# Optimization experiments

Measured on AMD Instinct MI355X. Metric: run time of the kernel, lower is better.

## Reference

```python
import jax, jax.numpy as jnp
import numpy as np

D_MODEL = 1024
NUM_HEADS = 16
D_K = D_MODEL // NUM_HEADS


def setup_inputs() -> dict:
    key = jax.random.key(0)
    ks = jax.random.split(key, 10)
    s = 1.0 / np.sqrt(D_MODEL)  # ~ torch Linear init scale
    inp = {
        "x": jax.random.normal(ks[0], (2, 2048, D_MODEL), dtype=jnp.float32),
        "Wq": jax.random.uniform(ks[1], (D_MODEL, D_MODEL), jnp.float32, -s, s),
        "bq": jax.random.uniform(ks[2], (D_MODEL,), jnp.float32, -s, s),
        "Wk": jax.random.uniform(ks[3], (D_MODEL, D_MODEL), jnp.float32, -s, s),
        "bk": jax.random.uniform(ks[4], (D_MODEL,), jnp.float32, -s, s),
        "Wv": jax.random.uniform(ks[5], (D_MODEL, D_MODEL), jnp.float32, -s, s),
        "bv": jax.random.uniform(ks[6], (D_MODEL,), jnp.float32, -s, s),
        "Wo": jax.random.uniform(ks[7], (D_MODEL, D_MODEL), jnp.float32, -s, s),
        "bo": jax.random.uniform(ks[8], (D_MODEL,), jnp.float32, -s, s),
        "ln_gamma": jnp.ones((D_MODEL,), jnp.float32),
        "ln_beta": jnp.zeros((D_MODEL,), jnp.float32),
    }
    return inp


def reference(x, Wq, bq, Wk, bk, Wv, bv, Wo, bo, ln_gamma, ln_beta):
    B, S, D = x.shape
    residual = x
    # LayerNorm (eps=1e-5 as torch default)
    mu = jnp.mean(x, axis=-1, keepdims=True)
    var = jnp.mean(jnp.square(x - mu), axis=-1, keepdims=True)
    xn = (x - mu) * jax.lax.rsqrt(var + 1e-5) * ln_gamma + ln_beta
    # QKV projections (torch Linear: y = x @ W^T + b) -> (B, H, S, d_k)
    def proj(W, b):
        return (xn @ W.T + b).reshape(B, S, NUM_HEADS, D_K).transpose(0, 2, 1, 3)
    Q, K, V = proj(Wq, bq), proj(Wk, bk), proj(Wv, bv)
    scores = jnp.einsum("bhqd,bhkd->bhqk", Q, K) / np.sqrt(D_K).astype(np.float32)
    attn = jax.nn.softmax(scores, axis=-1)  # (B, H, S, S); dropout is no-op (eval)
    context = jnp.einsum("bhqk,bhkd->bhqd", attn, V)
    context = context.transpose(0, 2, 1, 3).reshape(B, S, D)
    out = context @ Wo.T + bo
    return out + residual, attn.mean(axis=1)
```

## Files before the change

kernel.cpp:

```cpp
#include <hip/hip_runtime.h>
#include <stdint.h>
#include <stddef.h>

#define DEV static __device__ __forceinline__

typedef float f32x4 __attribute__((ext_vector_type(4)));
typedef float f32x16 __attribute__((ext_vector_type(16)));
typedef unsigned u32x4 __attribute__((ext_vector_type(4)));
typedef __bf16 bf16x8 __attribute__((ext_vector_type(8)));

DEV short f2bf(float f) {
  union { float f; unsigned u; } a; a.f = f;
  unsigned r = a.u + 0x7fffu + ((a.u >> 16) & 1u);
  return (short)(r >> 16);
}

DEV void gld_lds16(const void* g, void* lds) {
  __builtin_amdgcn_global_load_lds(
      (__attribute__((address_space(1))) void*)(void*)g,
      (__attribute__((address_space(3))) void*)lds, 16, 0, 0);
}

DEV f32x4 MFMA(bf16x8 a, bf16x8 b, f32x4 c) {
  return __builtin_amdgcn_mfma_f32_16x16x32_bf16(a, b, c, 0, 0, 0);
}
DEV f32x16 MFMA32(bf16x8 a, bf16x8 b, f32x16 c) {
  return __builtin_amdgcn_mfma_f32_32x32x16_bf16(a, b, c, 0, 0, 0);
}

DEV float ex2(float x) { return __builtin_amdgcn_exp2f(x); }

DEV unsigned cvtpk(float lo, float hi) {
  unsigned r;
  asm("v_cvt_pk_bf16_f32 %0, %1, %2" : "=v"(r) : "v"(lo), "v"(hi));
  return r;
}

DEV float xhalf_sum(float v) {
  float a = v, b = v;
  asm volatile("v_permlane32_swap_b32 %0, %1" : "+v"(a), "+v"(b));
  return a + b;
}

#define LOG2E 1.4426950408889634f


__global__ __launch_bounds__(256) void k_cvtw_ln(
    const float* __restrict__ w0, const float* __restrict__ w1,
    const float* __restrict__ w2, const float* __restrict__ w3,
    short* __restrict__ dst, const float* __restrict__ x,
    const float* __restrict__ g, const float* __restrict__ be,
    short* __restrict__ xn) {
  __shared__ float ps[4], pss[4];
  if (blockIdx.x < 4096) {
    int i = blockIdx.x * 256 + threadIdx.x;
    int sel = i >> 18;
    const float* src = sel == 0 ? w0 : sel == 1 ? w1 : sel == 2 ? w2 : w3;
    int off = (i & 0x3ffff) * 4;
    float4 v = *(const float4*)(src + off);
    short4 o4; o4.x = f2bf(v.x); o4.y = f2bf(v.y); o4.z = f2bf(v.z); o4.w = f2bf(v.w);
    *(short4*)(dst + (size_t)i * 4) = o4;
  } else {
    int row = blockIdx.x - 4096;
    int t = threadIdx.x;
    const float4* xr = (const float4*)(x + (size_t)row * 1024);
    float4 v = xr[t];
    float s = v.x + v.y + v.z + v.w;
    float ss = v.x * v.x + v.y * v.y + v.z * v.z + v.w * v.w;
#pragma unroll
    for (int o = 32; o; o >>= 1) { s += __shfl_down(s, o); ss += __shfl_down(ss, o); }
    int w = t >> 6, lane = t & 63;
    if (lane == 0) { ps[w] = s; pss[w] = ss; }
    __syncthreads();
    float st = ps[0] + ps[1] + ps[2] + ps[3];
    float sst = pss[0] + pss[1] + pss[2] + pss[3];
    float mean = st * (1.0f / 1024.0f);
    float var = sst * (1.0f / 1024.0f) - mean * mean;
    float rstd = rsqrtf(var + 1e-5f);
    float4 gv = ((const float4*)g)[t];
    float4 bv = ((const float4*)be)[t];
    short4 o4;
    o4.x = f2bf((v.x - mean) * rstd * gv.x + bv.x);
    o4.y = f2bf((v.y - mean) * rstd * gv.y + bv.y);
    o4.z = f2bf((v.z - mean) * rstd * gv.z + bv.z);
    o4.w = f2bf((v.w - mean) * rstd * gv.w + bv.w);
    ((short4*)(xn + (size_t)row * 1024))[t] = o4;
  }
}

__global__ __launch_bounds__(256) void k_gemm_qkv(
    const short* __restrict__ xn, const short* __restrict__ wbf,
    const float* __restrict__ bq, const float* __restrict__ bk,
    const float* __restrict__ bv, short* __restrict__ q_ws,
    short* __restrict__ k_ws, short* __restrict__ v_ws) {
  __shared__ __align__(16) short at[128 * 32];
  __shared__ __align__(16) short bt[128 * 32];
  int t = threadIdx.x, lane = t & 63, w = t >> 6;
  int wr = w >> 1, wc = w & 1;
  int z = blockIdx.z;
  int row0 = blockIdx.y * 128, col0 = blockIdx.x * 128;
  const short* A = xn + (size_t)row0 * 1024;
  const short* Bw = wbf + (size_t)z * (1024 * 1024) + (size_t)col0 * 1024;
  f32x4 acc[4][4];
#pragma unroll
  for (int m = 0; m < 4; m++)
#pragma unroll
    for (int n = 0; n < 4; n++) acc[m][n] = (f32x4)0.0f;

  for (int k0 = 0; k0 < 1024; k0 += 32) {
#pragma unroll
    for (int i = 0; i < 2; i++) {
      int c = t + i * 256;
      int r = c >> 2, cc = (c & 3) * 8;
      gld_lds16(A + (size_t)r * 1024 + k0 + cc, &at[c * 8]);
      gld_lds16(Bw + (size_t)r * 1024 + k0 + cc, &bt[c * 8]);
    }
    __syncthreads();
    bf16x8 af[4], bfr[4];
#pragma unroll
    for (int m = 0; m < 4; m++)
      af[m] = *(const bf16x8*)&at[(wr * 64 + m * 16 + (lane & 15)) * 32 + (lane >> 4) * 8];
#pragma unroll
    for (int n = 0; n < 4; n++)
      bfr[n] = *(const bf16x8*)&bt[(wc * 64 + n * 16 + (lane & 15)) * 32 + (lane >> 4) * 8];
#pragma unroll
    for (int m = 0; m < 4; m++)
#pragma unroll
      for (int n = 0; n < 4; n++) acc[m][n] = MFMA(af[m], bfr[n], acc[m][n]);
    __syncthreads();
  }
  const float* bias = z == 0 ? bq : z == 1 ? bk : bv;
  short* dst = z == 0 ? q_ws : z == 1 ? k_ws : v_ws;
  float scal = z == 0 ? (0.125f * LOG2E) : 1.0f;
#pragma unroll
  for (int m = 0; m < 4; m++)
#pragma unroll
    for (int n = 0; n < 4; n++)
#pragma unroll
      for (int r = 0; r < 4; r++) {
        int grow = row0 + wr * 64 + m * 16 + (lane >> 4) * 4 + r;
        int gcol = col0 + wc * 64 + n * 16 + (lane & 15);
        float val = (acc[m][n][r] + bias[gcol]) * scal;
        int bb = grow >> 11, s = grow & 2047, h = gcol >> 6, d = gcol & 63;
        dst[(((size_t)bb * 16 + h) * 2048 + s) * 64 + d] = f2bf(val);
      }
}

__global__ __launch_bounds__(256) void k_trv(const short* __restrict__ v_ws,
                                             short* __restrict__ vt_ws) {
  __shared__ short tile[64][65];
  int bh = blockIdx.y, s0 = blockIdx.x * 64;
  const short* src = v_ws + ((size_t)bh * 2048 + s0) * 64;
  int t = threadIdx.x;
#pragma unroll
  for (int i = 0; i < 4; i++) {
    int c = t + i * 256;
    int r = c >> 4, d4 = (c & 15) * 4;
    short4 v4 = *(const short4*)&src[r * 64 + d4];
    tile[d4 + 0][r] = v4.x; tile[d4 + 1][r] = v4.y;
    tile[d4 + 2][r] = v4.z; tile[d4 + 3][r] = v4.w;
  }
  __syncthreads();
#pragma unroll
  for (int i = 0; i < 4; i++) {
    int c = t + i * 256;
    int d = c >> 4, r4 = (c & 15) * 4;
    short4 o4;
    o4.x = tile[d][r4 + 0]; o4.y = tile[d][r4 + 1];
    o4.z = tile[d][r4 + 2]; o4.w = tile[d][r4 + 3];
    *(short4*)&vt_ws[((size_t)bh * 64 + d) * 2048 + s0 + r4] = o4;
  }
}

__global__ __launch_bounds__(256, 2) void k_attn1(
    const short* __restrict__ q_ws, const short* __restrict__ k_ws,
    const short* __restrict__ vt_ws, short* __restrict__ o_ws,
    float* __restrict__ l_ws) {
  __shared__ __align__(16) short k_lds[4][64 * 64];
  __shared__ __align__(16) short vt_lds[5][64 * 64];
  int t = threadIdx.x, lane = t & 63, w = t >> 6;
  int hi = lane >> 5, l31 = lane & 31;
  int qt = blockIdx.x, hd = blockIdx.y, b = blockIdx.z;
  int bh = b * 16 + hd;
  int q0 = qt * 128;
  const short* qb = q_ws + (size_t)bh * (2048 * 64);
  const short* kb = k_ws + (size_t)bh * (2048 * 64);
  const short* vtb = vt_ws + (size_t)bh * (64 * 2048);
  int qg = q0 + w * 32 + l31;

  bf16x8 qf[4];
#pragma unroll
  for (int d4 = 0; d4 < 4; d4++)
    qf[d4] = *(const bf16x8*)&qb[(size_t)qg * 64 + d4 * 16 + hi * 8];
  asm volatile("s_waitcnt vmcnt(0)" ::: "memory");

  const short *kp0, *kp1, *vp0, *vp1;
  {
    int c = t, r = c >> 3, j = (c & 7) ^ (r & 7);
    kp0 = kb + (size_t)r * 64 + j * 8;
    vp0 = vtb + (size_t)r * 2048 + j * 8;
  }
  {
    int c = t + 256, r = c >> 3, j = (c & 7) ^ (r & 7);
    kp1 = kb + (size_t)r * 64 + j * 8;
    vp1 = vtb + (size_t)r * 2048 + j * 8;
  }

  int koff[8];
#pragma unroll
  for (int d4 = 0; d4 < 4; d4++) {
    int row0 = l31, row1 = 32 + l31;
    koff[2 * d4]     = row0 * 64 + (((d4 * 2 + hi) ^ (row0 & 7)) * 8);
    koff[2 * d4 + 1] = row1 * 64 + (((d4 * 2 + hi) ^ (row1 & 7)) * 8);
  }

#define STG(tl_)                                                         \
  {                                                                      \
    gld_lds16(kp0 + (size_t)(tl_) * 4096, &k_lds[(tl_) & 3][t * 8]);     \
    gld_lds16(kp1 + (size_t)(tl_) * 4096, &k_lds[(tl_) & 3][(t + 256) * 8]); \
    gld_lds16(vp0 + (size_t)(tl_) * 64, &vt_lds[(tl_) % 5][t * 8]);      \
    gld_lds16(vp1 + (size_t)(tl_) * 64, &vt_lds[(tl_) % 5][(t + 256) * 8]); \
  }

  STG(0);
  STG(1);

  f32x16 Oacc[2];
#pragma unroll
  for (int i = 0; i < 16; i++) { Oacc[0][i] = 0.0f; Oacc[1][i] = 0.0f; }
  float lrun = 0.0f;
  bf16x8 pb[4];

  for (int it = 0; it < 32; ++it) {
    int tn = it + 2 <= 31 ? it + 2 : 31;
    STG(tn);
    asm volatile("s_waitcnt vmcnt(8)" ::: "memory");
    __builtin_amdgcn_s_barrier();

    const short* kl = k_lds[it & 3];
    const short* vl = vt_lds[(it + 4) % 5];

    bf16x8 kfr[8], vfr[8];
#pragma unroll
    for (int i = 0; i < 8; i++) kfr[i] = *(const bf16x8*)&kl[koff[i]];
#pragma unroll
    for (int i = 0; i < 8; i++) vfr[i] = *(const bf16x8*)&vl[koff[i]];

    __builtin_amdgcn_s_setprio(1);
    f32x16 S0 = (f32x16)0.0f, S1 = (f32x16)0.0f;
#pragma unroll
    for (int d4 = 0; d4 < 4; d4++) {
      S0 = MFMA32(kfr[2 * d4], qf[d4], S0);
      S1 = MFMA32(kfr[2 * d4 + 1], qf[d4], S1);
    }
    if (it) {
#pragma unroll
      for (int ks = 0; ks < 4; ks++) {
        Oacc[0] = MFMA32(vfr[2 * ks], pb[ks], Oacc[0]);
        Oacc[1] = MFMA32(vfr[2 * ks + 1], pb[ks], Oacc[1]);
      }
    }
    __builtin_amdgcn_s_setprio(0);

    float rs0 = 0.0f, rs1 = 0.0f;
#pragma unroll
    for (int i = 0; i < 16; i++) {
      float p0 = ex2(S0[i]);
      float p1 = ex2(S1[i]);
      S0[i] = p0; S1[i] = p1;
      rs0 += p0; rs1 += p1;
    }
    lrun += xhalf_sum(rs0 + rs1);

#pragma unroll
    for (int ks = 0; ks < 4; ks++) {
      unsigned wA, wB, wC, wD;
      if (ks == 0) {
        wA = cvtpk(S0[0], S0[1]);  wB = cvtpk(S0[2], S0[3]);
        wC = cvtpk(S0[4], S0[5]);  wD = cvtpk(S0[6], S0[7]);
      } else if (ks == 1) {
        wA = cvtpk(S0[8], S0[9]);  wB = cvtpk(S0[10], S0[11]);
        wC = cvtpk(S0[12], S0[13]); wD = cvtpk(S0[14], S0[15]);
      } else if (ks == 2) {
        wA = cvtpk(S1[0], S1[1]);  wB = cvtpk(S1[2], S1[3]);
        wC = cvtpk(S1[4], S1[5]);  wD = cvtpk(S1[6], S1[7]);
      } else {
        wA = cvtpk(S1[8], S1[9]);  wB = cvtpk(S1[10], S1[11]);
        wC = cvtpk(S1[12], S1[13]); wD = cvtpk(S1[14], S1[15]);
      }
      asm volatile("v_permlane32_swap_b32 %0, %1" : "+v"(wA), "+v"(wC));
      asm volatile("v_permlane32_swap_b32 %0, %1" : "+v"(wB), "+v"(wD));
      u32x4 uu; uu.x = wA; uu.y = wB; uu.z = wC; uu.w = wD;
      pb[ks] = __builtin_bit_cast(bf16x8, uu);
    }
  }
  asm volatile("s_waitcnt vmcnt(0)" ::: "memory");
  __builtin_amdgcn_s_barrier();

  {
    const short* vl = vt_lds[1];
    __builtin_amdgcn_s_setprio(1);
#pragma unroll
    for (int ks = 0; ks < 4; ks++) {
      Oacc[0] = MFMA32(*(const bf16x8*)&vl[koff[2 * ks]], pb[ks], Oacc[0]);
      Oacc[1] = MFMA32(*(const bf16x8*)&vl[koff[2 * ks + 1]], pb[ks], Oacc[1]);
    }
    __builtin_amdgcn_s_setprio(0);
  }

  float rl = 1.0f / lrun;
  if (lane < 32) {
    l_ws[bh * 2048 + qg] = rl;
  }
#pragma unroll
  for (int dt = 0; dt < 2; dt++)
#pragma unroll
    for (int g = 0; g < 4; g++) {
      short4 o4;
      o4.x = f2bf(Oacc[dt][g * 4 + 0] * rl);
      o4.y = f2bf(Oacc[dt][g * 4 + 1] * rl);
      o4.z = f2bf(Oacc[dt][g * 4 + 2] * rl);
      o4.w = f2bf(Oacc[dt][g * 4 + 3] * rl);
      int d = dt * 32 + g * 8 + hi * 4;
      *(short4*)&o_ws[((size_t)(b * 2048 + qg)) * 1024 + hd * 64 + d] = o4;
    }
}

__global__ __launch_bounds__(256, 3) void k_attn2(
    const short* __restrict__ q_ws, const short* __restrict__ k_ws,
    const float* __restrict__ l_ws, float* __restrict__ out1) {
  __shared__ __align__(16) short k_lds2[3][128 * 64];
  __shared__ __align__(16) float l_lds[3][64];
  int t = threadIdx.x, lane = t & 63, w = t >> 6;
  int k2 = blockIdx.x * 128, q0 = blockIdx.y * 64, b = blockIdx.z;

  f32x4 pacc[8];
#pragma unroll
  for (int n = 0; n < 8; n++) pacc[n] = (f32x4)0.0f;

  int qrow = q0 + w * 16 + (lane & 15);
  size_t qoff0 = (size_t)qrow * 64 + (lane >> 4) * 8;
  const short* qb0 = q_ws + (size_t)(b * 16) * (2048 * 64);

#define STAGE2(hh)                                                               \
  {                                                                              \
    int bh_ = b * 16 + (hh);                                                     \
    const short* kb_ = k_ws + (size_t)bh_ * (2048 * 64);                         \
    _Pragma("unroll")                                                            \
    for (int i = 0; i < 4; i++) {                                                \
      int c = t + i * 256;                                                       \
      int r = c >> 3, j = (c & 7) ^ (r & 7);                                     \
      gld_lds16(kb_ + (size_t)(k2 + r) * 64 + j * 8, &k_lds2[(hh) % 3][c * 8]);  \
    }                                                                            \
    int cc = w * 4 + (t & 63);                                                   \
    if ((t & 63) < 4) {                                                          \
      gld_lds16(&l_ws[(size_t)bh_ * 2048 + q0 + cc * 4], &l_lds[(hh) % 3][cc * 4]); \
    }                                                                            \
  }

  STAGE2(0);
  for (int h = 0; h < 16; ++h) {
    bf16x8 qf0 = *(const bf16x8*)&qb0[(size_t)h * (2048 * 64) + qoff0];
    bf16x8 qf1 = *(const bf16x8*)&qb0[(size_t)h * (2048 * 64) + qoff0 + 32];
    int hn = h < 15 ? h + 1 : 15;
    STAGE2(hn);
    asm volatile("s_waitcnt vmcnt(5)" ::: "memory");
    __builtin_amdgcn_s_barrier();

    const short* kl = k_lds2[h % 3];
    f32x4 sc[8];
#pragma unroll
    for (int n = 0; n < 8; n++) sc[n] = (f32x4)0.0f;
#pragma unroll
    for (int kf = 0; kf < 2; kf++)
#pragma unroll
      for (int n = 0; n < 8; n++) {
        int row = n * 16 + (lane & 15);
        bf16x8 kfr = *(const bf16x8*)&kl[row * 64 + (((kf * 4 + (lane >> 4)) ^ (row & 7)) * 8)];
        sc[n] = MFMA(kf == 0 ? qf0 : qf1, kfr, sc[n]);
      }
    f32x4 lh = *(const f32x4*)&l_lds[h % 3][w * 16 + (lane >> 4) * 4];
#pragma unroll
    for (int n = 0; n < 8; n++)
#pragma unroll
      for (int r = 0; r < 4; r++)
        pacc[n][r] += ex2(sc[n][r]) * lh[r];
  }

#pragma unroll
  for (int n = 0; n < 8; n++)
#pragma unroll
    for (int r = 0; r < 4; r++) {
      int q = q0 + w * 16 + (lane >> 4) * 4 + r;
      int k = k2 + n * 16 + (lane & 15);
      out1[((size_t)b * 2048 + q) * 2048 + k] = pacc[n][r] * 0.0625f;
    }
}

__global__ __launch_bounds__(256) void k_gemm_out(
    const short* __restrict__ o_ws, const short* __restrict__ wo_bf,
    const float* __restrict__ bo, const float* __restrict__ x,
    float* __restrict__ out0) {
  __shared__ __align__(16) short at[128 * 32];
  __shared__ __align__(16) short bt[128 * 32];
  int t = threadIdx.x, lane = t & 63, w = t >> 6;
  int wr = w >> 1, wc = w & 1;
  int row0 = blockIdx.y * 128, col0 = blockIdx.x * 128;
  const short* A = o_ws + (size_t)row0 * 1024;
  const short* Bw = wo_bf + (size_t)col0 * 1024;
  f32x4 acc[4][4];
#pragma unroll
  for (int m = 0; m < 4; m++)
#pragma unroll
    for (int n = 0; n < 4; n++) acc[m][n] = (f32x4)0.0f;

  for (int k0 = 0; k0 < 1024; k0 += 32) {
#pragma unroll
    for (int i = 0; i < 2; i++) {
      int c = t + i * 256;
      int r = c >> 2, cc = (c & 3) * 8;
      gld_lds16(A + (size_t)r * 1024 + k0 + cc, &at[c * 8]);
      gld_lds16(Bw + (size_t)r * 1024 + k0 + cc, &bt[c * 8]);
    }
    __syncthreads();
    bf16x8 af[4], bfr[4];
#pragma unroll
    for (int m = 0; m < 4; m++)
      af[m] = *(const bf16x8*)&at[(wr * 64 + m * 16 + (lane & 15)) * 32 + (lane >> 4) * 8];
#pragma unroll
    for (int n = 0; n < 4; n++)
      bfr[n] = *(const bf16x8*)&bt[(wc * 64 + n * 16 + (lane & 15)) * 32 + (lane >> 4) * 8];
#pragma unroll
    for (int m = 0; m < 4; m++)
#pragma unroll
      for (int n = 0; n < 4; n++) acc[m][n] = MFMA(af[m], bfr[n], acc[m][n]);
    __syncthreads();
  }
#pragma unroll
  for (int m = 0; m < 4; m++)
#pragma unroll
    for (int n = 0; n < 4; n++)
#pragma unroll
      for (int r = 0; r < 4; r++) {
        int grow = row0 + wr * 64 + m * 16 + (lane >> 4) * 4 + r;
        int gcol = col0 + wc * 64 + n * 16 + (lane & 15);
        float val = acc[m][n][r] + bo[gcol] + x[(size_t)grow * 1024 + gcol];
        out0[(size_t)grow * 1024 + gcol] = val;
      }
}

extern "C" void kernel_launch(void* const* d_in, const int* in_sizes, int n_in,
                              void* d_out, int out_size, void* d_ws, size_t ws_size,
                              hipStream_t stream) {
  (void)in_sizes; (void)n_in; (void)out_size; (void)ws_size;
  const float* x   = (const float*)d_in[0];
  const float* Wq  = (const float*)d_in[1];
  const float* bq  = (const float*)d_in[2];
  const float* Wk  = (const float*)d_in[3];
  const float* bk  = (const float*)d_in[4];
  const float* Wv  = (const float*)d_in[5];
  const float* bv  = (const float*)d_in[6];
  const float* Wo  = (const float*)d_in[7];
  const float* bo  = (const float*)d_in[8];
  const float* lng = (const float*)d_in[9];
  const float* lnb = (const float*)d_in[10];
  float* out0 = (float*)d_out;
  float* out1 = out0 + (size_t)2 * 2048 * 1024;

  char* ws = (char*)d_ws;
  short* xn    = (short*)(ws);
  short* q_ws  = (short*)(ws + 8388608);
  short* k_ws  = (short*)(ws + 16777216);
  short* o_ws  = (short*)(ws + 25165824);
  short* vt_ws = (short*)(ws + 33554432);
  short* wbf   = (short*)(ws + 41943040);
  float* l_ws  = (float*)(ws + 50331648);

  k_cvtw_ln<<<8192, 256, 0, stream>>>(Wq, Wk, Wv, Wo, wbf, x, lng, lnb, xn);
  k_gemm_qkv<<<dim3(8, 32, 3), 256, 0, stream>>>(xn, wbf, bq, bk, bv, q_ws, k_ws, o_ws);
  k_trv<<<dim3(32, 32), 256, 0, stream>>>(o_ws, vt_ws);
  k_attn1<<<dim3(16, 16, 2), 256, 0, stream>>>(q_ws, k_ws, vt_ws, o_ws, l_ws);
  k_attn2<<<dim3(16, 32, 2), 256, 0, stream>>>(q_ws, k_ws, l_ws, out1);
  k_gemm_out<<<dim3(8, 32), 256, 0, stream>>>(o_ws, wbf + (size_t)3 * 1024 * 1024, bo, x, out0);
}
```

Before: 160.7 us.

## Process two 32-row query slices per wave in attention kernel to reuse K/V tiles

Each wave in k_attn1 now handles 64 query rows (two 32-row slices) instead of 32, so each block covers 256 queries and the grid halves. Each K/V tile loaded into LDS and registers feeds twice as many MFMAs, which cuts LDS traffic and global K/V reloads per query. The softmax/pack of slice A is placed between the MFMA bursts so it can overlap with slice B. In exchange, register use doubles, launch bounds drop to one block per CU, and only 256 blocks are launched, which lowers occupancy and latency hiding.

After: 171.6 us. 6.8% more time.

```diff
diff --git a/kernel.cpp b/kernel.cpp
--- a/kernel.cpp
+++ b/kernel.cpp
@@ -172,7 +172,7 @@
   }
 }
 
-__global__ __launch_bounds__(256, 2) void k_attn1(
+__global__ __launch_bounds__(256, 1) void k_attn1(
     const short* __restrict__ q_ws, const short* __restrict__ k_ws,
     const short* __restrict__ vt_ws, short* __restrict__ o_ws,
     float* __restrict__ l_ws) {
@@ -182,16 +182,19 @@
   int hi = lane >> 5, l31 = lane & 31;
   int qt = blockIdx.x, hd = blockIdx.y, b = blockIdx.z;
   int bh = b * 16 + hd;
-  int q0 = qt * 128;
+  int q0 = qt * 256;
   const short* qb = q_ws + (size_t)bh * (2048 * 64);
   const short* kb = k_ws + (size_t)bh * (2048 * 64);
   const short* vtb = vt_ws + (size_t)bh * (64 * 2048);
-  int qg = q0 + w * 32 + l31;
-
-  bf16x8 qf[4];
-#pragma unroll
-  for (int d4 = 0; d4 < 4; d4++)
-    qf[d4] = *(const bf16x8*)&qb[(size_t)qg * 64 + d4 * 16 + hi * 8];
+  int qg0 = q0 + w * 64 + l31;
+  int qg1 = qg0 + 32;
+
+  bf16x8 qfa[4], qfb[4];
+#pragma unroll
+  for (int d4 = 0; d4 < 4; d4++) {
+    qfa[d4] = *(const bf16x8*)&qb[(size_t)qg0 * 64 + d4 * 16 + hi * 8];
+    qfb[d4] = *(const bf16x8*)&qb[(size_t)qg1 * 64 + d4 * 16 + hi * 8];
+  }
   asm volatile("s_waitcnt vmcnt(0)" ::: "memory");
 
   const short *kp0, *kp1, *vp0, *vp1;
@@ -225,11 +228,48 @@
   STG(0);
   STG(1);
 
-  f32x16 Oacc[2];
-#pragma unroll
-  for (int i = 0; i < 16; i++) { Oacc[0][i] = 0.0f; Oacc[1][i] = 0.0f; }
-  float lrun = 0.0f;
-  bf16x8 pb[4];
+  f32x16 OaccA[2], OaccB[2];
+#pragma unroll
+  for (int i = 0; i < 16; i++) {
+    OaccA[0][i] = 0.0f; OaccA[1][i] = 0.0f;
+    OaccB[0][i] = 0.0f; OaccB[1][i] = 0.0f;
+  }
+  float lrunA = 0.0f, lrunB = 0.0f;
+  bf16x8 pba[4], pbb[4];
+
+#define SMPACK(S0, S1, pb, lrun)                                          \
+  {                                                                       \
+    float rs0 = 0.0f, rs1 = 0.0f;                                         \
+    _Pragma("unroll")                                                     \
+    for (int i = 0; i < 16; i++) {                                        \
+      float p0 = ex2(S0[i]);                                              \
+      float p1 = ex2(S1[i]);                                              \
+      S0[i] = p0; S1[i] = p1;                                             \
+      rs0 += p0; rs1 += p1;                                               \
+    }                                                                     \
+    lrun += xhalf_sum(rs0 + rs1);                                         \
+    _Pragma("unroll")                                                     \
+    for (int ks = 0; ks < 4; ks++) {                                      \
+      unsigned wA, wB, wC, wD;                                            \
+      if (ks == 0) {                                                      \
+        wA = cvtpk(S0[0], S0[1]);  wB = cvtpk(S0[2], S0[3]);              \
+        wC = cvtpk(S0[4], S0[5]);  wD = cvtpk(S0[6], S0[7]);              \
+      } else if (ks == 1) {                                               \
+        wA = cvtpk(S0[8], S0[9]);  wB = cvtpk(S0[10], S0[11]);            \
+        wC = cvtpk(S0[12], S0[13]); wD = cvtpk(S0[14], S0[15]);           \
+      } else if (ks == 2) {                                               \
+        wA = cvtpk(S1[0], S1[1]);  wB = cvtpk(S1[2], S1[3]);              \
+        wC = cvtpk(S1[4], S1[5]);  wD = cvtpk(S1[6], S1[7]);              \
+      } else {                                                            \
+        wA = cvtpk(S1[8], S1[9]);  wB = cvtpk(S1[10], S1[11]);            \
+        wC = cvtpk(S1[12], S1[13]); wD = cvtpk(S1[14], S1[15]);           \
+      }                                                                   \
+      asm volatile("v_permlane32_swap_b32 %0, %1" : "+v"(wA), "+v"(wC));  \
+      asm volatile("v_permlane32_swap_b32 %0, %1" : "+v"(wB), "+v"(wD));  \
+      u32x4 uu; uu.x = wA; uu.y = wB; uu.z = wC; uu.w = wD;               \
+      pb[ks] = __builtin_bit_cast(bf16x8, uu);                            \
+    }                                                                     \
+  }
 
   for (int it = 0; it < 32; ++it) {
     int tn = it + 2 <= 31 ? it + 2 : 31;
@@ -247,52 +287,38 @@
     for (int i = 0; i < 8; i++) vfr[i] = *(const bf16x8*)&vl[koff[i]];
 
     __builtin_amdgcn_s_setprio(1);
-    f32x16 S0 = (f32x16)0.0f, S1 = (f32x16)0.0f;
+    f32x16 Sa0 = (f32x16)0.0f, Sa1 = (f32x16)0.0f;
 #pragma unroll
     for (int d4 = 0; d4 < 4; d4++) {
-      S0 = MFMA32(kfr[2 * d4], qf[d4], S0);
-      S1 = MFMA32(kfr[2 * d4 + 1], qf[d4], S1);
+      Sa0 = MFMA32(kfr[2 * d4], qfa[d4], Sa0);
+      Sa1 = MFMA32(kfr[2 * d4 + 1], qfa[d4], Sa1);
     }
     if (it) {
 #pragma unroll
       for (int ks = 0; ks < 4; ks++) {
-        Oacc[0] = MFMA32(vfr[2 * ks], pb[ks], Oacc[0]);
-        Oacc[1] = MFMA32(vfr[2 * ks + 1], pb[ks], Oacc[1]);
+        OaccA[0] = MFMA32(vfr[2 * ks], pba[ks], OaccA[0]);
+        OaccA[1] = MFMA32(vfr[2 * ks + 1], pba[ks], OaccA[1]);
       }
+#pragma unroll
+      for (int ks = 0; ks < 4; ks++) {
+        OaccB[0] = MFMA32(vfr[2 * ks], pbb[ks], OaccB[0]);
+        OaccB[1] = MFMA32(vfr[2 * ks + 1], pbb[ks], OaccB[1]);
+      }
     }
     __builtin_amdgcn_s_setprio(0);
 
-    float rs0 = 0.0f, rs1 = 0.0f;
-#pragma unroll
-    for (int i = 0; i < 16; i++) {
-      float p0 = ex2(S0[i]);
-      float p1 = ex2(S1[i]);
-      S0[i] = p0; S1[i] = p1;
-      rs0 += p0; rs1 += p1;
-    }
-    lrun += xhalf_sum(rs0 + rs1);
-
-#pragma unroll
-    for (int ks = 0; ks < 4; ks++) {
-      unsigned wA, wB, wC, wD;
-      if (ks == 0) {
-        wA = cvtpk(S0[0], S0[1]);  wB = cvtpk(S0[2], S0[3]);
-        wC = cvtpk(S0[4], S0[5]);  wD = cvtpk(S0[6], S0[7]);
-      } else if (ks == 1) {
-        wA = cvtpk(S0[8], S0[9]);  wB = cvtpk(S0[10], S0[11]);
-        wC = cvtpk(S0[12], S0[13]); wD = cvtpk(S0[14], S0[15]);
-      } else if (ks == 2) {
-        wA = cvtpk(S1[0], S1[1]);  wB = cvtpk(S1[2], S1[3]);
-        wC = cvtpk(S1[4], S1[5]);  wD = cvtpk(S1[6], S1[7]);
-      } else {
-        wA = cvtpk(S1[8], S1[9]);  wB = cvtpk(S1[10], S1[11]);
-        wC = cvtpk(S1[12], S1[13]); wD = cvtpk(S1[14], S1[15]);
-      }
-      asm volatile("v_permlane32_swap_b32 %0, %1" : "+v"(wA), "+v"(wC));
-      asm volatile("v_permlane32_swap_b32 %0, %1" : "+v"(wB), "+v"(wD));
-      u32x4 uu; uu.x = wA; uu.y = wB; uu.z = wC; uu.w = wD;
-      pb[ks] = __builtin_bit_cast(bf16x8, uu);
-    }
+    SMPACK(Sa0, Sa1, pba, lrunA);
+
+    __builtin_amdgcn_s_setprio(1);
+    f32x16 Sb0 = (f32x16)0.0f, Sb1 = (f32x16)0.0f;
+#pragma unroll
+    for (int d4 = 0; d4 < 4; d4++) {
+      Sb0 = MFMA32(kfr[2 * d4], qfb[d4], Sb0);
+      Sb1 = MFMA32(kfr[2 * d4 + 1], qfb[d4], Sb1);
+    }
+    __builtin_amdgcn_s_setprio(0);
+
+    SMPACK(Sb0, Sb1, pbb, lrunB);
   }
   asm volatile("s_waitcnt vmcnt(0)" ::: "memory");
   __builtin_amdgcn_s_barrier();
@@ -302,27 +328,37 @@
     __builtin_amdgcn_s_setprio(1);
 #pragma unroll
     for (int ks = 0; ks < 4; ks++) {
-      Oacc[0] = MFMA32(*(const bf16x8*)&vl[koff[2 * ks]], pb[ks], Oacc[0]);
-      Oacc[1] = MFMA32(*(const bf16x8*)&vl[koff[2 * ks + 1]], pb[ks], Oacc[1]);
+      bf16x8 v0 = *(const bf16x8*)&vl[koff[2 * ks]];
+      bf16x8 v1 = *(const bf16x8*)&vl[koff[2 * ks + 1]];
+      OaccA[0] = MFMA32(v0, pba[ks], OaccA[0]);
+      OaccA[1] = MFMA32(v1, pba[ks], OaccA[1]);
+      OaccB[0] = MFMA32(v0, pbb[ks], OaccB[0]);
+      OaccB[1] = MFMA32(v1, pbb[ks], OaccB[1]);
     }
     __builtin_amdgcn_s_setprio(0);
   }
 
-  float rl = 1.0f / lrun;
+  float rlA = 1.0f / lrunA, rlB = 1.0f / lrunB;
   if (lane < 32) {
-    l_ws[bh * 2048 + qg] = rl;
+    l_ws[bh * 2048 + qg0] = rlA;
+    l_ws[bh * 2048 + qg1] = rlB;
   }
 #pragma unroll
   for (int dt = 0; dt < 2; dt++)
 #pragma unroll
     for (int g = 0; g < 4; g++) {
+      int d = dt * 32 + g * 8 + hi * 4;
       short4 o4;
-      o4.x = f2bf(Oacc[dt][g * 4 + 0] * rl);
-      o4.y = f2bf(Oacc[dt][g * 4 + 1] * rl);
-      o4.z = f2bf(Oacc[dt][g * 4 + 2] * rl);
-      o4.w = f2bf(Oacc[dt][g * 4 + 3] * rl);
-      int d = dt * 32 + g * 8 + hi * 4;
-      *(short4*)&o_ws[((size_t)(b * 2048 + qg)) * 1024 + hd * 64 + d] = o4;
+      o4.x = f2bf(OaccA[dt][g * 4 + 0] * rlA);
+      o4.y = f2bf(OaccA[dt][g * 4 + 1] * rlA);
+      o4.z = f2bf(OaccA[dt][g * 4 + 2] * rlA);
+      o4.w = f2bf(OaccA[dt][g * 4 + 3] * rlA);
+      *(short4*)&o_ws[((size_t)(b * 2048 + qg0)) * 1024 + hd * 64 + d] = o4;
+      o4.x = f2bf(OaccB[dt][g * 4 + 0] * rlB);
+      o4.y = f2bf(OaccB[dt][g * 4 + 1] * rlB);
+      o4.z = f2bf(OaccB[dt][g * 4 + 2] * rlB);
+      o4.w = f2bf(OaccB[dt][g * 4 + 3] * rlB);
+      *(short4*)&o_ws[((size_t)(b * 2048 + qg1)) * 1024 + hd * 64 + d] = o4;
     }
 }
 
@@ -479,7 +515,7 @@
   k_cvtw_ln<<<8192, 256, 0, stream>>>(Wq, Wk, Wv, Wo, wbf, x, lng, lnb, xn);
   k_gemm_qkv<<<dim3(8, 32, 3), 256, 0, stream>>>(xn, wbf, bq, bk, bv, q_ws, k_ws, o_ws);
   k_trv<<<dim3(32, 32), 256, 0, stream>>>(o_ws, vt_ws);
-  k_attn1<<<dim3(16, 16, 2), 256, 0, stream>>>(q_ws, k_ws, vt_ws, o_ws, l_ws);
+  k_attn1<<<dim3(8, 16, 2), 256, 0, stream>>>(q_ws, k_ws, vt_ws, o_ws, l_ws);
   k_attn2<<<dim3(16, 32, 2), 256, 0, stream>>>(q_ws, k_ws, l_ws, out1);
   k_gemm_out<<<dim3(8, 32), 256, 0, stream>>>(o_ws, wbf + (size_t)3 * 1024 * 1024, bo, x, out0);
 }
```
